# Optimization experiments

Hardware: AMD Instinct MI355X
Metric: run time of the kernel (lower is better)

## Reference

```python
import jax, jax.numpy as jnp
import numpy as np

T, N, H = 256, 64, 512
DT, GAMMA, EPS = 0.01, 1.0, 1.0

def setup_inputs() -> dict:
    key = jax.random.key(0)
    ks = jax.random.split(key, 6)
    s = 1.0 / np.sqrt(H)  # keep recurrent dynamics stable
    return {
        "x": jax.random.normal(ks[0], (T, N, H), jnp.float32),
        "connection_matrix": (jax.random.uniform(ks[1], (N, N)) < 0.5).astype(jnp.float32),
        "W_h": jax.random.normal(ks[2], (N, H, H), jnp.float32) * s,
        "W_x": jax.random.normal(ks[3], (N, H, H), jnp.float32) * s,
        "b": jax.random.normal(ks[4], (N, H), jnp.float32) * 0.1,
        "initial_states": jnp.zeros((N, 2, H), jnp.float32),
    }

def reference(x, connection_matrix, W_h, W_x, b, initial_states):
    # x: (T, N, H); states: (N, 2, H) with states[:,0] = h_y (the archetype output)
    def step(carry, x_t):
        states, outs = carry
        # message passing: mix previous outputs through the connection matrix,
        # then gate with the external input (elementwise)
        new_ins = (connection_matrix @ outs) * x_t                      # (N, H)
        hy, hz = states[:, 0], states[:, 1]
        # batched RON cell over all N archetypes
        pre = (jnp.einsum('nij,nj->ni', W_h, hy)
               + jnp.einsum('nij,nj->ni', W_x, new_ins) + b)            # (N, H)
        hz_n = hz + DT * (jnp.tanh(pre) - GAMMA * hy - EPS * hz)
        hy_n = hy + DT * hz_n
        new_states = jnp.stack([hy_n, hz_n], axis=1)                    # (N, 2, H)
        return (new_states, hy_n), (new_states, new_ins)

    init_outs = jnp.zeros_like(x[0])  # initial_outs=None path in the original
    _, (states_seq, ins_seq) = jax.lax.scan(step, (initial_states, init_outs), x)
    # original prepends the initial state and x[0] to the returned lists
    states_all = jnp.concatenate([initial_states[None], states_seq], axis=0)  # (T+1, N, 2, H)
    ins_all = jnp.concatenate([x[:1], ins_seq], axis=0)                       # (T+1, N, H)
    return states_all, ins_all
```

## Files before the change

### kernel.cpp

```cpp
#include <hip/hip_runtime.h>
#include <hip/hip_cooperative_groups.h>

namespace cg = cooperative_groups;

constexpr int   T_     = 256;
constexpr int   N_     = 64;
constexpr int   H_     = 512;
constexpr float DT_    = 0.01f;
constexpr float GAMMA_ = 1.0f;
constexpr float EPS_   = 1.0f;

constexpr int GRID  = 2048;
constexpr int BLOCK = 256;
constexpr int WGPN  = GRID / N_;
constexpr int ROWS  = H_ / WGPN;

__device__ __forceinline__ void step_body(
    int t, int n, int q, int tid, int lane, int wave,
    const float* __restrict__ x,
    const float* __restrict__ W_h, const float* __restrict__ W_x,
    float* __restrict__ states_all, float* __restrict__ ins_all,
    float* s_hy, float* s_ins, float* s_pre,
    const float* s_conn, const float* s_bias)
{
    const float* st_t = states_all + (size_t)t * N_ * 2 * H_;
    const float* xt   = x + (size_t)t * N_ * H_;

    {
        const int h0 = tid, h1 = tid + 256;
        float i0 = 0.f, i1 = 0.f;
        if (t > 0) {
            float a0 = 0.f, a1 = 0.f;
            #pragma unroll 8
            for (int m = 0; m < N_; ++m) {
                const float c   = s_conn[m];
                const float* hm = st_t + m * 2 * H_;
                a0 += c * hm[h0];
                a1 += c * hm[h1];
            }
            i0 = a0 * xt[n * H_ + h0];
            i1 = a1 * xt[n * H_ + h1];
        }
        s_ins[h0] = i0;
        s_ins[h1] = i1;
        s_hy[h0] = st_t[n * 2 * H_ + h0];
        s_hy[h1] = st_t[n * 2 * H_ + h1];
        float* insd = ins_all + (size_t)(t + 1) * N_ * H_ + n * H_;
        if (h0 / ROWS == q) insd[h0] = i0;
        if (h1 / ROWS == q) insd[h1] = i1;
    }
    __syncthreads();

    {
        const float4* vh = (const float4*)s_hy;
        const float4* vi = (const float4*)s_ins;
        for (int rl = wave; rl < ROWS; rl += 4) {
            const int i = q * ROWS + rl;
            const float4* wh = (const float4*)(W_h + ((size_t)n * H_ + i) * H_);
            const float4* wx = (const float4*)(W_x + ((size_t)n * H_ + i) * H_);
            float acc = 0.f;
            #pragma unroll
            for (int k = 0; k < 2; ++k) {
                const float4 a = wh[k * 64 + lane];
                const float4 v = vh[k * 64 + lane];
                acc += a.x * v.x + a.y * v.y + a.z * v.z + a.w * v.w;
                const float4 c4 = wx[k * 64 + lane];
                const float4 u = vi[k * 64 + lane];
                acc += c4.x * u.x + c4.y * u.y + c4.z * u.z + c4.w * u.w;
            }
            #pragma unroll
            for (int off = 32; off; off >>= 1)
                acc += __shfl_xor(acc, off);
            if (lane == 0) s_pre[rl] = acc;
        }
    }
    __syncthreads();

    if (tid < ROWS) {
        const int i   = q * ROWS + tid;
        const float pre  = s_pre[tid] + s_bias[tid];
        const float hy   = st_t[n * 2 * H_ + i];
        const float hz   = st_t[n * 2 * H_ + H_ + i];
        const float th   = tanhf(pre);
        const float hz_n = hz + DT_ * (th - GAMMA_ * hy - EPS_ * hz);
        const float hy_n = hy + DT_ * hz_n;
        float* st1 = states_all + (size_t)(t + 1) * N_ * 2 * H_ + n * 2 * H_;
        st1[i]      = hy_n;
        st1[H_ + i] = hz_n;
    }
}

__global__ __launch_bounds__(BLOCK, 8)
void archetypes_persistent(const float* __restrict__ x,
                           const float* __restrict__ conn,
                           const float* __restrict__ W_h,
                           const float* __restrict__ W_x,
                           const float* __restrict__ bias,
                           const float* __restrict__ init_states,
                           float* __restrict__ out)
{
    cg::grid_group grid = cg::this_grid();

    const int tid  = threadIdx.x;
    const int wg   = blockIdx.x;
    const int n    = wg / WGPN;
    const int q    = wg % WGPN;
    const int lane = tid & 63;
    const int wave = tid >> 6;

    float* states_all = out;
    float* ins_all    = out + (size_t)(T_ + 1) * N_ * 2 * H_;

    __shared__ float s_hy[H_];
    __shared__ float s_ins[H_];
    __shared__ float s_pre[ROWS];
    __shared__ float s_conn[N_];
    __shared__ float s_bias[ROWS];

    if (tid < N_)   s_conn[tid] = conn[n * N_ + tid];
    if (tid < ROWS) s_bias[tid] = bias[n * H_ + q * ROWS + tid];

    for (int idx = wg * BLOCK + tid; idx < N_ * 2 * H_; idx += GRID * BLOCK)
        states_all[idx] = init_states[idx];
    for (int idx = wg * BLOCK + tid; idx < N_ * H_; idx += GRID * BLOCK)
        ins_all[idx] = x[idx];

    grid.sync();

    for (int t = 0; t < T_; ++t) {
        step_body(t, n, q, tid, lane, wave, x, W_h, W_x,
                  states_all, ins_all, s_hy, s_ins, s_pre, s_conn, s_bias);
        grid.sync();
    }
}

__global__ __launch_bounds__(BLOCK)
void archetypes_init(const float* __restrict__ x,
                     const float* __restrict__ init_states,
                     float* __restrict__ out)
{
    float* states_all = out;
    float* ins_all    = out + (size_t)(T_ + 1) * N_ * 2 * H_;
    const int idx = blockIdx.x * BLOCK + threadIdx.x;
    if (idx < N_ * 2 * H_) states_all[idx] = init_states[idx];
    if (idx < N_ * H_)     ins_all[idx]    = x[idx];
}

__global__ __launch_bounds__(BLOCK)
void archetypes_step(int t,
                     const float* __restrict__ x,
                     const float* __restrict__ conn,
                     const float* __restrict__ W_h,
                     const float* __restrict__ W_x,
                     const float* __restrict__ bias,
                     float* __restrict__ out)
{
    const int tid  = threadIdx.x;
    const int wg   = blockIdx.x;
    const int n    = wg / WGPN;
    const int q    = wg % WGPN;
    const int lane = tid & 63;
    const int wave = tid >> 6;

    float* states_all = out;
    float* ins_all    = out + (size_t)(T_ + 1) * N_ * 2 * H_;

    __shared__ float s_hy[H_];
    __shared__ float s_ins[H_];
    __shared__ float s_pre[ROWS];
    __shared__ float s_conn[N_];
    __shared__ float s_bias[ROWS];

    if (tid < N_)   s_conn[tid] = conn[n * N_ + tid];
    if (tid < ROWS) s_bias[tid] = bias[n * H_ + q * ROWS + tid];
    __syncthreads();

    step_body(t, n, q, tid, lane, wave, x, W_h, W_x,
              states_all, ins_all, s_hy, s_ins, s_pre, s_conn, s_bias);
}

extern "C" void kernel_launch(void* const* d_in, const int* in_sizes, int n_in,
                              void* d_out, int out_size, void* d_ws, size_t ws_size,
                              hipStream_t stream) {
    const float* x     = (const float*)d_in[0];
    const float* conn  = (const float*)d_in[1];
    const float* W_h   = (const float*)d_in[2];
    const float* W_x   = (const float*)d_in[3];
    const float* bias  = (const float*)d_in[4];
    const float* inits = (const float*)d_in[5];
    float*       outp  = (float*)d_out;

    int perCU = 0;
    (void)hipOccupancyMaxActiveBlocksPerMultiprocessor(
        &perCU, (const void*)archetypes_persistent, BLOCK, 0);
    const bool coop_ok = (perCU * 256 >= GRID);

    if (coop_ok) {
        void* args[] = {(void*)&x, (void*)&conn, (void*)&W_h, (void*)&W_x,
                        (void*)&bias, (void*)&inits, (void*)&outp};
        hipLaunchCooperativeKernel((void*)archetypes_persistent,
                                   dim3(GRID), dim3(BLOCK), args, 0, stream);
    } else {
        archetypes_init<<<dim3((N_ * 2 * H_ + BLOCK - 1) / BLOCK), dim3(BLOCK),
                          0, stream>>>(x, inits, outp);
        for (int t = 0; t < T_; ++t)
            archetypes_step<<<dim3(GRID), dim3(BLOCK), 0, stream>>>(
                t, x, conn, W_h, W_x, bias, outp);
    }
}
```

Measured before the change: 7.099 ms.

## Keep W_h slice in registers and part of W_x in LDS across timesteps

Halves the persistent grid to 1024 workgroups (4 per CU) so each workgroup owns 32 rows. Its W_h rows stay in registers for the whole time loop and the first 16 W_x rows sit in shared memory, so those weights are no longer re-read from global/L2 on every step. The remaining W_x rows are still streamed from global memory. The cost is much higher register and LDS use per workgroup and fewer workgroups, which may hurt latency hiding or the cooperative-launch occupancy check.

```diff
diff --git a/kernel.cpp b/kernel.cpp
--- a/kernel.cpp
+++ b/kernel.cpp
@@ -10,87 +10,14 @@
 constexpr float GAMMA_ = 1.0f;
 constexpr float EPS_   = 1.0f;
 
-constexpr int GRID  = 2048;
+constexpr int GRID  = 1024;
 constexpr int BLOCK = 256;
 constexpr int WGPN  = GRID / N_;
 constexpr int ROWS  = H_ / WGPN;
-
-__device__ __forceinline__ void step_body(
-    int t, int n, int q, int tid, int lane, int wave,
-    const float* __restrict__ x,
-    const float* __restrict__ W_h, const float* __restrict__ W_x,
-    float* __restrict__ states_all, float* __restrict__ ins_all,
-    float* s_hy, float* s_ins, float* s_pre,
-    const float* s_conn, const float* s_bias)
-{
-    const float* st_t = states_all + (size_t)t * N_ * 2 * H_;
-    const float* xt   = x + (size_t)t * N_ * H_;
-
-    {
-        const int h0 = tid, h1 = tid + 256;
-        float i0 = 0.f, i1 = 0.f;
-        if (t > 0) {
-            float a0 = 0.f, a1 = 0.f;
-            #pragma unroll 8
-            for (int m = 0; m < N_; ++m) {
-                const float c   = s_conn[m];
-                const float* hm = st_t + m * 2 * H_;
-                a0 += c * hm[h0];
-                a1 += c * hm[h1];
-            }
-            i0 = a0 * xt[n * H_ + h0];
-            i1 = a1 * xt[n * H_ + h1];
-        }
-        s_ins[h0] = i0;
-        s_ins[h1] = i1;
-        s_hy[h0] = st_t[n * 2 * H_ + h0];
-        s_hy[h1] = st_t[n * 2 * H_ + h1];
-        float* insd = ins_all + (size_t)(t + 1) * N_ * H_ + n * H_;
-        if (h0 / ROWS == q) insd[h0] = i0;
-        if (h1 / ROWS == q) insd[h1] = i1;
-    }
-    __syncthreads();
-
-    {
-        const float4* vh = (const float4*)s_hy;
-        const float4* vi = (const float4*)s_ins;
-        for (int rl = wave; rl < ROWS; rl += 4) {
-            const int i = q * ROWS + rl;
-            const float4* wh = (const float4*)(W_h + ((size_t)n * H_ + i) * H_);
-            const float4* wx = (const float4*)(W_x + ((size_t)n * H_ + i) * H_);
-            float acc = 0.f;
-            #pragma unroll
-            for (int k = 0; k < 2; ++k) {
-                const float4 a = wh[k * 64 + lane];
-                const float4 v = vh[k * 64 + lane];
-                acc += a.x * v.x + a.y * v.y + a.z * v.z + a.w * v.w;
-                const float4 c4 = wx[k * 64 + lane];
-                const float4 u = vi[k * 64 + lane];
-                acc += c4.x * u.x + c4.y * u.y + c4.z * u.z + c4.w * u.w;
-            }
-            #pragma unroll
-            for (int off = 32; off; off >>= 1)
-                acc += __shfl_xor(acc, off);
-            if (lane == 0) s_pre[rl] = acc;
-        }
-    }
-    __syncthreads();
-
-    if (tid < ROWS) {
-        const int i   = q * ROWS + tid;
-        const float pre  = s_pre[tid] + s_bias[tid];
-        const float hy   = st_t[n * 2 * H_ + i];
-        const float hz   = st_t[n * 2 * H_ + H_ + i];
-        const float th   = tanhf(pre);
-        const float hz_n = hz + DT_ * (th - GAMMA_ * hy - EPS_ * hz);
-        const float hy_n = hy + DT_ * hz_n;
-        float* st1 = states_all + (size_t)(t + 1) * N_ * 2 * H_ + n * 2 * H_;
-        st1[i]      = hy_n;
-        st1[H_ + i] = hz_n;
-    }
-}
-
-__global__ __launch_bounds__(BLOCK, 8)
+constexpr int RPW   = ROWS / 4;
+constexpr int LROWS = 16;
+
+__global__ __launch_bounds__(BLOCK, 4)
 void archetypes_persistent(const float* __restrict__ x,
                            const float* __restrict__ conn,
                            const float* __restrict__ W_h,
@@ -116,7 +43,23 @@
     __shared__ float s_pre[ROWS];
     __shared__ float s_conn[N_];
     __shared__ float s_bias[ROWS];
-
+    __shared__ float s_wx[LROWS][H_];
+
+    const float4* Wh4 = (const float4*)(W_h + ((size_t)n * H_ + q * ROWS) * H_);
+    const float4* Wx4 = (const float4*)(W_x + ((size_t)n * H_ + q * ROWS) * H_);
+    float4 wh_reg[RPW][2];
+    #pragma unroll
+    for (int j = 0; j < RPW; ++j) {
+        const int r_l = wave + 4 * j;
+        #pragma unroll
+        for (int k = 0; k < 2; ++k)
+            wh_reg[j][k] = Wh4[r_l * (H_ / 4) + k * 64 + lane];
+    }
+    {
+        float4* dst = (float4*)&s_wx[0][0];
+        for (int idx = tid; idx < LROWS * H_ / 4; idx += BLOCK)
+            dst[idx] = Wx4[idx];
+    }
     if (tid < N_)   s_conn[tid] = conn[n * N_ + tid];
     if (tid < ROWS) s_bias[tid] = bias[n * H_ + q * ROWS + tid];
 
@@ -128,8 +71,78 @@
     grid.sync();
 
     for (int t = 0; t < T_; ++t) {
-        step_body(t, n, q, tid, lane, wave, x, W_h, W_x,
-                  states_all, ins_all, s_hy, s_ins, s_pre, s_conn, s_bias);
+        const float* st_t = states_all + (size_t)t * N_ * 2 * H_;
+
+        {
+            const int h0 = tid, h1 = tid + 256;
+            float i0 = 0.f, i1 = 0.f;
+            if (t > 0) {
+                const float* xr = x + (size_t)t * N_ * H_ + n * H_;
+                float a0 = 0.f, a1 = 0.f;
+                #pragma unroll 8
+                for (int m = 0; m < N_; ++m) {
+                    const float c = s_conn[m];
+                    a0 += c * st_t[m * 2 * H_ + h0];
+                    a1 += c * st_t[m * 2 * H_ + h1];
+                }
+                i0 = a0 * xr[h0];
+                i1 = a1 * xr[h1];
+            }
+            s_ins[h0] = i0;
+            s_ins[h1] = i1;
+            s_hy[h0] = st_t[n * 2 * H_ + h0];
+            s_hy[h1] = st_t[n * 2 * H_ + h1];
+            float* insd = ins_all + (size_t)(t + 1) * N_ * H_ + n * H_;
+            if (h0 / ROWS == q) insd[h0] = i0;
+            if (h1 / ROWS == q) insd[h1] = i1;
+        }
+        __syncthreads();
+
+        {
+            const float4* vh = (const float4*)s_hy;
+            const float4* vi = (const float4*)s_ins;
+            const float4 v0 = vh[lane], v1 = vh[64 + lane];
+            const float4 u0 = vi[lane], u1 = vi[64 + lane];
+            #pragma unroll
+            for (int j = 0; j < RPW; ++j) {
+                const int r_l = wave + 4 * j;
+                float4 wx0, wx1;
+                if (j < 4) {
+                    const float4* lx = (const float4*)&s_wx[r_l][0];
+                    wx0 = lx[lane];
+                    wx1 = lx[64 + lane];
+                } else {
+                    wx0 = Wx4[r_l * (H_ / 4) + lane];
+                    wx1 = Wx4[r_l * (H_ / 4) + 64 + lane];
+                }
+                float acc = 0.f;
+                acc += wh_reg[j][0].x * v0.x + wh_reg[j][0].y * v0.y +
+                       wh_reg[j][0].z * v0.z + wh_reg[j][0].w * v0.w;
+                acc += wx0.x * u0.x + wx0.y * u0.y + wx0.z * u0.z + wx0.w * u0.w;
+                acc += wh_reg[j][1].x * v1.x + wh_reg[j][1].y * v1.y +
+                       wh_reg[j][1].z * v1.z + wh_reg[j][1].w * v1.w;
+                acc += wx1.x * u1.x + wx1.y * u1.y + wx1.z * u1.z + wx1.w * u1.w;
+                #pragma unroll
+                for (int off = 32; off; off >>= 1)
+                    acc += __shfl_xor(acc, off);
+                if (lane == 0) s_pre[r_l] = acc;
+            }
+        }
+        __syncthreads();
+
+        if (tid < ROWS) {
+            const int i   = q * ROWS + tid;
+            const float pre  = s_pre[tid] + s_bias[tid];
+            const float hy   = st_t[n * 2 * H_ + i];
+            const float hz   = st_t[n * 2 * H_ + H_ + i];
+            const float th   = tanhf(pre);
+            const float hz_n = hz + DT_ * (th - GAMMA_ * hy - EPS_ * hz);
+            const float hy_n = hy + DT_ * hz_n;
+            float* st1 = states_all + (size_t)(t + 1) * N_ * 2 * H_ + n * 2 * H_;
+            st1[i]      = hy_n;
+            st1[H_ + i] = hz_n;
+        }
+
         grid.sync();
     }
 }
@@ -175,8 +188,69 @@
     if (tid < ROWS) s_bias[tid] = bias[n * H_ + q * ROWS + tid];
     __syncthreads();
 
-    step_body(t, n, q, tid, lane, wave, x, W_h, W_x,
-              states_all, ins_all, s_hy, s_ins, s_pre, s_conn, s_bias);
+    const float* st_t = states_all + (size_t)t * N_ * 2 * H_;
+    {
+        const int h0 = tid, h1 = tid + 256;
+        float i0 = 0.f, i1 = 0.f;
+        if (t > 0) {
+            const float* xr = x + (size_t)t * N_ * H_ + n * H_;
+            float a0 = 0.f, a1 = 0.f;
+            #pragma unroll 8
+            for (int m = 0; m < N_; ++m) {
+                const float c = s_conn[m];
+                a0 += c * st_t[m * 2 * H_ + h0];
+                a1 += c * st_t[m * 2 * H_ + h1];
+            }
+            i0 = a0 * xr[h0];
+            i1 = a1 * xr[h1];
+        }
+        s_ins[h0] = i0;
+        s_ins[h1] = i1;
+        s_hy[h0] = st_t[n * 2 * H_ + h0];
+        s_hy[h1] = st_t[n * 2 * H_ + h1];
+        float* insd = ins_all + (size_t)(t + 1) * N_ * H_ + n * H_;
+        if (h0 / ROWS == q) insd[h0] = i0;
+        if (h1 / ROWS == q) insd[h1] = i1;
+    }
+    __syncthreads();
+    {
+        const float4* vh = (const float4*)s_hy;
+        const float4* vi = (const float4*)s_ins;
+        const float4* Wh4 = (const float4*)(W_h + ((size_t)n * H_ + q * ROWS) * H_);
+        const float4* Wx4 = (const float4*)(W_x + ((size_t)n * H_ + q * ROWS) * H_);
+        const float4 v0 = vh[lane], v1 = vh[64 + lane];
+        const float4 u0 = vi[lane], u1 = vi[64 + lane];
+        #pragma unroll
+        for (int j = 0; j < RPW; ++j) {
+            const int r_l = wave + 4 * j;
+            const float4 a0 = Wh4[r_l * (H_ / 4) + lane];
+            const float4 a1 = Wh4[r_l * (H_ / 4) + 64 + lane];
+            const float4 wx0 = Wx4[r_l * (H_ / 4) + lane];
+            const float4 wx1 = Wx4[r_l * (H_ / 4) + 64 + lane];
+            float acc = 0.f;
+            acc += a0.x * v0.x + a0.y * v0.y + a0.z * v0.z + a0.w * v0.w;
+            acc += wx0.x * u0.x + wx0.y * u0.y + wx0.z * u0.z + wx0.w * u0.w;
+            acc += a1.x * v1.x + a1.y * v1.y + a1.z * v1.z + a1.w * v1.w;
+            acc += wx1.x * u1.x + wx1.y * u1.y + wx1.z * u1.z + wx1.w * u1.w;
+            #pragma unroll
+            for (int off = 32; off; off >>= 1)
+                acc += __shfl_xor(acc, off);
+            if (lane == 0) s_pre[r_l] = acc;
+        }
+    }
+    __syncthreads();
+    if (tid < ROWS) {
+        const int i   = q * ROWS + tid;
+        const float pre  = s_pre[tid] + s_bias[tid];
+        const float hy   = st_t[n * 2 * H_ + i];
+        const float hz   = st_t[n * 2 * H_ + H_ + i];
+        const float th   = tanhf(pre);
+        const float hz_n = hz + DT_ * (th - GAMMA_ * hy - EPS_ * hz);
+        const float hy_n = hy + DT_ * hz_n;
+        float* st1 = states_all + (size_t)(t + 1) * N_ * 2 * H_ + n * 2 * H_;
+        st1[i]      = hy_n;
+        st1[H_ + i] = hz_n;
+    }
 }
 
 extern "C" void kernel_launch(void* const* d_in, const int* in_sizes, int n_in,
```

Result: faster. 6.792 ms (-4.3%).
